# Kernel tuning notes

Hardware: AMD Instinct MI355X
Metric: run time of the kernel (lower is better)

## Reference

```python
import jax, jax.numpy as jnp
import numpy as np

B, N, FD = 2, 50000, 13
E = 250000
M, H = 128, 128          # message_dim, hidden_dim
EDGE_IN = 2 * FD + 8     # 34
NODE_IN = FD + 2 * M     # 269


def _mlp(x, w1, b1, w2, b2):
    return jnp.tanh(x @ w1 + b1) @ w2 + b2


def setup_inputs() -> dict:
    root = jax.random.key(0)
    k = lambda i: jax.random.fold_in(root, i)

    def lin(i, din, dout):
        w = jax.random.normal(k(i), (din, dout), jnp.float32) * np.float32(1.0 / np.sqrt(din))
        b = jax.random.normal(k(i + 100), (dout,), jnp.float32) * np.float32(0.01)
        return w, b

    ew1, eb1 = lin(1, EDGE_IN, H); ew2, eb2 = lin(2, H, M)      # mlp_edge
    ww1, wb1 = lin(3, EDGE_IN, H); ww2, wb2 = lin(4, H, 1)      # mlp_weight
    xw1, xb1 = lin(5, EDGE_IN, H); xw2, xb2 = lin(6, H, M)      # mlp_edge_world
    yw1, yb1 = lin(7, EDGE_IN, H); yw2, yb2 = lin(8, H, 1)      # mlp_weight_world
    nw1, nb1 = lin(9, NODE_IN, H); nw2, nb2 = lin(10, H, FD)    # mlp_node

    z_h = jax.random.normal(k(20), (B, N, FD), jnp.float32)
    edge_hh = jax.random.randint(k(21), (B, 2, E), 0, N, jnp.int32)
    edge_world = jax.random.randint(k(22), (B, 2, E), 0, N, jnp.int32)
    return dict(z_h=z_h, edge_hh=edge_hh, edge_world=edge_world,
                ew1=ew1, eb1=eb1, ew2=ew2, eb2=eb2,
                ww1=ww1, wb1=wb1, ww2=ww2, wb2=wb2,
                xw1=xw1, xb1=xb1, xw2=xw2, xb2=xb2,
                yw1=yw1, yb1=yb1, yw2=yw2, yb2=yb2,
                nw1=nw1, nb1=nb1, nw2=nw2, nb2=nb2)


def _edge_features(z, s, t):
    # z: (N, FD); s, t: (E,)
    pos, vel = z[:, 0:3], z[:, 3:6]
    diff = pos[s] - pos[t]                               # (E, 3)
    dist = jnp.sum(diff * diff, axis=-1, keepdims=True)  # (E, 1) squared distance
    vxc = jnp.cross(vel[s], vel[t])                      # (E, 3)
    vxn = jnp.linalg.norm(vxc, axis=-1, keepdims=True)   # (E, 1)
    return jnp.concatenate([diff, dist, vxc, vxn], axis=-1)  # (E, 8)


def reference(z_h, edge_hh, edge_world,
              ew1, eb1, ew2, eb2, ww1, wb1, ww2, wb2,
              xw1, xb1, xw2, xb2, yw1, yb1, yw2, yb2,
              nw1, nb1, nw2, nb2):
    n_nodes = z_h.shape[1]

    def per_batch(z, e_hh, e_w):
        # normal edges
        s, t = e_hh[0], e_hh[1]
        inp = jnp.concatenate([z[s], z[t], _edge_features(z, s, t)], axis=-1)  # (E, 34)
        m = _mlp(inp, ew1, eb1, ew2, eb2)                                       # (E, M)
        w = jax.nn.sigmoid(_mlp(inp, ww1, wb1, ww2, wb2))                       # (E, 1)
        agg_h = jnp.zeros((n_nodes, M), z.dtype).at[t].add(w * m)
        # world edges
        sw, tw = e_w[0], e_w[1]
        inpw = jnp.concatenate([z[sw], z[tw], _edge_features(z, sw, tw)], axis=-1)
        mw = _mlp(inpw, xw1, xb1, xw2, xb2)
        ww_ = jax.nn.sigmoid(_mlp(inpw, yw1, yb1, yw2, yb2))
        agg_w = jnp.zeros((n_nodes, M), z.dtype).at[tw].add(ww_ * mw)
        return agg_h, agg_w

    m_agg_h, m_agg_w = jax.vmap(per_batch)(z_h, edge_hh, edge_world)  # (B, N, M) each
    input_node = jnp.concatenate([z_h, m_agg_h, m_agg_w], axis=-1)    # (B, N, 269)
    delta_z_h = _mlp(input_node, nw1, nb1, nw2, nb2)                  # (B, N, 13)
    return delta_z_h
```

## Files before the change

kernel.cpp:

```cpp
#include <hip/hip_runtime.h>
#include <hip/hip_bf16.h>

#define B_   2
#define N_   50000
#define FD_  13
#define E_   250000
#define M_   128
#define H_   128

typedef __attribute__((ext_vector_type(8))) short  short8;
typedef __attribute__((ext_vector_type(8))) __bf16 bf16x8;
typedef __attribute__((ext_vector_type(4))) float  f32x4;
typedef __attribute__((ext_vector_type(4))) unsigned int uint4v;
typedef __attribute__((ext_vector_type(8))) unsigned short ushort8;

#define AGG_BYTES  (4ull * N_ * 128 * 4)
#define HIST_BYTES (4ull * N_ * 4)
#define SORT_BYTES (4ull * E_ * 4)
#define OFF_EW1 0u
#define OFF_WW1 8192u
#define OFF_EW2 16384u
#define OFF_XW1 32768u
#define OFF_YW1 40960u
#define OFF_XW2 49152u
#define OFF_NW1 65536u
#define OFF_NW2 102400u

__device__ __forceinline__ float bf2f(unsigned short u) {
    unsigned int v = ((unsigned int)u) << 16;
    return __builtin_bit_cast(float, v);
}
__device__ __forceinline__ unsigned short f2bf(float f) {
    __bf16 h = (__bf16)f;
    return __builtin_bit_cast(unsigned short, h);
}
__device__ __forceinline__ float tanh_fast(float x) {
    float e = __expf(x + x);
    float r = __builtin_amdgcn_rcpf(e + 1.0f);
    return __builtin_fmaf(-2.0f, r, 1.0f);
}
__device__ __forceinline__ float sigmoid_fast(float x) {
    return __builtin_amdgcn_rcpf(1.0f + __expf(-x));
}
__device__ __forceinline__ f32x4 mfma16(short8 a, short8 b, f32x4 c) {
    return __builtin_amdgcn_mfma_f32_16x16x32_bf16(
        __builtin_bit_cast(bf16x8, a), __builtin_bit_cast(bf16x8, b), c, 0, 0, 0);
}

__global__ void prep_kernel(const float* __restrict__ ew1, const float* __restrict__ ww1,
                            const float* __restrict__ ew2, const float* __restrict__ xw1,
                            const float* __restrict__ yw1, const float* __restrict__ xw2,
                            const float* __restrict__ nw1, const float* __restrict__ nw2,
                            unsigned short* __restrict__ fb, uint4v* __restrict__ hist4) {
    int m = blockIdx.y, f = blockIdx.x, l = threadIdx.x;
    {
        unsigned int flat = ((unsigned int)m * gridDim.x + (unsigned int)f) * 64u + (unsigned int)l;
        const uint4v zv = {0u, 0u, 0u, 0u};
        for (unsigned int i = flat; i < 50000u; i += gridDim.x * gridDim.y * 64u)
            hist4[i] = zv;
    }
    const float* src; int K, Nn, KS; unsigned int off;
    switch (m) {
        case 0: src = ew1; K = 34;  Nn = 128; KS = 2; off = OFF_EW1; break;
        case 1: src = ww1; K = 34;  Nn = 128; KS = 2; off = OFF_WW1; break;
        case 2: src = ew2; K = 128; Nn = 128; KS = 4; off = OFF_EW2; break;
        case 3: src = xw1; K = 34;  Nn = 128; KS = 2; off = OFF_XW1; break;
        case 4: src = yw1; K = 34;  Nn = 128; KS = 2; off = OFF_YW1; break;
        case 5: src = xw2; K = 128; Nn = 128; KS = 4; off = OFF_XW2; break;
        case 6: src = nw1; K = 269; Nn = 128; KS = 9; off = OFF_NW1; break;
        default: src = nw2; K = 128; Nn = 13; KS = 4; off = OFF_NW2; break;
    }
    int NT = (Nn + 15) / 16;
    if (f >= KS * NT) return;
    int ks = f / NT, nt = f % NT;
    int n = nt * 16 + (l & 15);
    unsigned short* dst = fb + off + ((unsigned int)f * 64u + (unsigned int)l) * 8u;
    #pragma unroll
    for (int j = 0; j < 8; j++) {
        int k = ks * 32 + ((l >> 4) * 8) + j;
        int kk = k; bool valid = (k < K) && (n < Nn);
        if (m == 6) {
            if (k < 256)      kk = k + 13;
            else if (k < 269) kk = k - 256;
            else              valid = false;
            valid = valid && (n < Nn);
        }
        dst[j] = valid ? f2bf(src[kk * Nn + n]) : (unsigned short)0;
    }
}

__global__ void hist_kernel(const int* __restrict__ ehh, const int* __restrict__ eww,
                            int* __restrict__ hist) {
    int p = blockIdx.y, idx = blockIdx.x * 256 + threadIdx.x;
    if (idx >= E_) return;
    const int* eg = ((p >> 1) ? eww : ehh) + (size_t)(p & 1) * 2 * E_;
    atomicAdd(&hist[p * N_ + eg[E_ + idx]], 1);
}

__global__ void scan_kernel(int* __restrict__ hist) {
    __shared__ int part[1024];
    const int p = blockIdx.x, tid = threadIdx.x;
    int* h = hist + p * N_;
    const int lo = tid * 52;
    int cnt = N_ - lo; if (cnt < 0) cnt = 0; if (cnt > 52) cnt = 52;
    int v[52];
    int sum = 0;
    if (cnt == 52) {
        const int4* src = (const int4*)(h + lo);
        #pragma unroll
        for (int i = 0; i < 13; i++) {
            int4 t = src[i];
            v[4*i] = t.x; v[4*i+1] = t.y; v[4*i+2] = t.z; v[4*i+3] = t.w;
        }
        #pragma unroll
        for (int i = 0; i < 52; i++) sum += v[i];
    } else {
        for (int i = 0; i < cnt; i++) sum += h[lo + i];
    }
    part[tid] = sum;
    __syncthreads();
    for (int off = 1; off < 1024; off <<= 1) {
        int t = (tid >= off) ? part[tid - off] : 0;
        __syncthreads();
        part[tid] += t;
        __syncthreads();
    }
    int excl = (tid == 0) ? 0 : part[tid - 1];
    if (cnt == 52) {
        int4* dst = (int4*)(h + lo);
        #pragma unroll
        for (int i = 0; i < 13; i++) {
            int4 o;
            o.x = excl; excl += v[4*i];
            o.y = excl; excl += v[4*i+1];
            o.z = excl; excl += v[4*i+2];
            o.w = excl; excl += v[4*i+3];
            dst[i] = o;
        }
    } else {
        for (int i = 0; i < cnt; i++) { int t = h[lo + i]; h[lo + i] = excl; excl += t; }
    }
}

__global__ void scatter_kernel(const int* __restrict__ ehh, const int* __restrict__ eww,
                               int* __restrict__ hist, unsigned int* __restrict__ sorted,
                               uint4v* __restrict__ agg4) {
    int p = blockIdx.y, idx = blockIdx.x * 256 + threadIdx.x;
    {
        unsigned int flat = ((unsigned int)p * gridDim.x + (unsigned int)blockIdx.x) * 256u
                          + (unsigned int)threadIdx.x;
        const unsigned int nthr = gridDim.x * gridDim.y * 256u;
        const uint4v zv = {0u, 0u, 0u, 0u};
        for (unsigned int i = flat; i < 6400000u; i += nthr) agg4[i] = zv;
    }
    if (idx >= E_) return;
    const int* eg = ((p >> 1) ? eww : ehh) + (size_t)(p & 1) * 2 * E_;
    int s = eg[idx];
    int t = eg[E_ + idx];
    int pos = atomicAdd(&hist[p * N_ + t], 1);
    sorted[(size_t)p * E_ + pos] = (unsigned int)s | ((unsigned int)t << 16);
}

__launch_bounds__(256, 3)
__global__ void edge_kernel_agg(const float* __restrict__ z,
                                const unsigned int* __restrict__ sorted,
                                const unsigned short* __restrict__ fb,
                                float* __restrict__ agg,
                                const float* __restrict__ eb1, const float* __restrict__ wb1,
                                const float* __restrict__ ww2, const float* __restrict__ wb2,
                                const float* __restrict__ eb2,
                                const float* __restrict__ xb1, const float* __restrict__ yb1,
                                const float* __restrict__ yw2, const float* __restrict__ yb2,
                                const float* __restrict__ xb2) {
    __shared__ alignas(16) unsigned short Abuf[128][48];
    __shared__ alignas(16) unsigned short Hbuf[128][136];
    __shared__ float w_acc[128];
    __shared__ int   tgt_s[128];

    const int tid  = threadIdx.x;
    const int lane = tid & 63, wv = tid >> 6, quad = lane >> 4, c = lane & 15;
    const int pass = blockIdx.y, b = pass & 1, set = pass >> 1;
    const int ebase = blockIdx.x * 128;

    const float* zb = z + (size_t)b * N_ * FD_;
    float* aggp = agg + (size_t)pass * N_ * 128;

    const short8* Fm1 = (const short8*)(fb + (set ? OFF_XW1 : OFF_EW1));
    const short8* Fw1 = (const short8*)(fb + (set ? OFF_YW1 : OFF_WW1));
    const short8* Fm2 = (const short8*)(fb + (set ? OFF_XW2 : OFF_EW2));
    const float* B1m = set ? xb1 : eb1;
    const float* B1w = set ? yb1 : wb1;
    const float* B2m = set ? xb2 : eb2;
    const float* Wv2 = set ? yw2 : ww2;
    const float wbias = (set ? yb2 : wb2)[0];

    const int nt0 = wv * 2;
    short8 bm[2][2], bw[2][2], b2f[2][4];
    float bias1m[2], bias1w[2], bias2m[2], w2v[2];
    #pragma unroll
    for (int i = 0; i < 2; i++) {
        int nt = nt0 + i, n = nt * 16 + c;
        #pragma unroll
        for (int ks = 0; ks < 2; ks++) { bm[i][ks] = Fm1[(ks * 8 + nt) * 64 + lane];
                                         bw[i][ks] = Fw1[(ks * 8 + nt) * 64 + lane]; }
        #pragma unroll
        for (int ks = 0; ks < 4; ks++) { b2f[i][ks] = Fm2[(ks * 8 + nt) * 64 + lane]; }
        bias1m[i] = B1m[n]; bias1w[i] = B1w[n];
        bias2m[i] = B2m[n]; w2v[i] = Wv2[n];
    }

    if (tid < 128) {
        const int e = tid;
        const int prt = e >> 4, pqd = (e >> 2) & 3, prr = e & 3;
        const int wpos = pqd * 32 + prt * 4 + prr;
        int sp = ebase + wpos;
        const bool valid = (sp < E_);
        if (!valid) sp = E_ - 1;
        unsigned int st = sorted[(size_t)pass * E_ + sp];
        int s = (int)(st & 0xffffu), t = (int)(st >> 16);
        tgt_s[e] = valid ? t : -1;
        w_acc[e] = 0.0f;
        const float* zs = zb + (size_t)s * 13;
        const float* zt = zb + (size_t)t * 13;
        float fs[13], ft[13];
        __builtin_memcpy(fs, zs, 13 * sizeof(float));
        __builtin_memcpy(ft, zt, 13 * sizeof(float));
        float d0 = fs[0] - ft[0], d1 = fs[1] - ft[1], d2 = fs[2] - ft[2];
        float dist = d0 * d0 + d1 * d1 + d2 * d2;
        float c0 = fs[4] * ft[5] - fs[5] * ft[4];
        float c1 = fs[5] * ft[3] - fs[3] * ft[5];
        float c2 = fs[3] * ft[4] - fs[4] * ft[3];
        float vxn = sqrtf(c0 * c0 + c1 * c1 + c2 * c2);
        unsigned short row[40];
        #pragma unroll
        for (int j = 0; j < 13; j++) { row[j] = f2bf(fs[j]); row[13 + j] = f2bf(ft[j]); }
        row[26] = f2bf(d0); row[27] = f2bf(d1); row[28] = f2bf(d2); row[29] = f2bf(dist);
        row[30] = f2bf(c0); row[31] = f2bf(c1); row[32] = f2bf(c2); row[33] = f2bf(vxn);
        #pragma unroll
        for (int j = 34; j < 40; j++) row[j] = 0;
        #pragma unroll
        for (int v = 0; v < 5; v++) {
            short8 sv;
            #pragma unroll
            for (int j = 0; j < 8; j++) sv[j] = (short)row[v * 8 + j];
            *((short8*)&Abuf[e][v * 8]) = sv;
        }
    }
    __syncthreads();

    #pragma unroll 1
    for (int rt = 0; rt < 8; rt++) {
        const unsigned short* ar = &Abuf[rt * 16 + c][0];
        short8 a0 = *((const short8*)(ar + quad * 8));
        short8 a1 = {};
        if (quad == 0) a1 = *((const short8*)(ar + 32));
        float wpart[4] = {0.f, 0.f, 0.f, 0.f};
        #pragma unroll
        for (int i = 0; i < 2; i++) {
            f32x4 accm = {bias1m[i], bias1m[i], bias1m[i], bias1m[i]};
            f32x4 accw = {bias1w[i], bias1w[i], bias1w[i], bias1w[i]};
            accm = mfma16(a0, bm[i][0], accm);
            accm = mfma16(a1, bm[i][1], accm);
            accw = mfma16(a0, bw[i][0], accw);
            accw = mfma16(a1, bw[i][1], accw);
            int n = (nt0 + i) * 16 + c;
            #pragma unroll
            for (int r = 0; r < 4; r++) {
                Hbuf[rt * 16 + quad * 4 + r][n] = f2bf(tanh_fast(accm[r]));
                wpart[r] += tanh_fast(accw[r]) * w2v[i];
            }
        }
        #pragma unroll
        for (int r = 0; r < 4; r++) {
            float v = wpart[r];
            v += __shfl_xor(v, 1); v += __shfl_xor(v, 2);
            v += __shfl_xor(v, 4); v += __shfl_xor(v, 8);
            if (c == r) atomicAdd(&w_acc[rt * 16 + quad * 4 + r], v);
        }
    }
    __syncthreads();
    if (tid < 128) w_acc[tid] = sigmoid_fast(w_acc[tid] + wbias);
    __syncthreads();

    {
        const int n0 = nt0 * 16 + c;
        const int n1 = n0 + 16;
        int   tp = -1;
        float va0 = 0.f, va1 = 0.f;
        bool  from_start = true;
        #pragma unroll 1
        for (int rt = 0; rt < 8; rt++) {
            const unsigned short* hr = &Hbuf[rt * 16 + c][0];
            short8 h0 = *((const short8*)(hr + quad * 8));
            short8 h1 = *((const short8*)(hr + 32 + quad * 8));
            short8 h2 = *((const short8*)(hr + 64 + quad * 8));
            short8 h3 = *((const short8*)(hr + 96 + quad * 8));
            f32x4 accA = {bias2m[0], bias2m[0], bias2m[0], bias2m[0]};
            f32x4 accB = {bias2m[1], bias2m[1], bias2m[1], bias2m[1]};
            accA = mfma16(h0, b2f[0][0], accA);
            accA = mfma16(h1, b2f[0][1], accA);
            accA = mfma16(h2, b2f[0][2], accA);
            accA = mfma16(h3, b2f[0][3], accA);
            accB = mfma16(h0, b2f[1][0], accB);
            accB = mfma16(h1, b2f[1][1], accB);
            accB = mfma16(h2, b2f[1][2], accB);
            accB = mfma16(h3, b2f[1][3], accB);
            const int elq = rt * 16 + quad * 4;
            #pragma unroll
            for (int r = 0; r < 4; r++) {
                const int row = elq + r;
                const int tg = tgt_s[row];
                const float g = w_acc[row];
                const float v0 = accA[r] * g;
                const float v1 = accB[r] * g;
                if (tg == tp) {
                    va0 += v0; va1 += v1;
                } else {
                    if (tp >= 0) {
                        float* dst = aggp + (size_t)tp * 128;
                        if (from_start) { atomicAdd(dst + n0, va0); atomicAdd(dst + n1, va1); }
                        else            { dst[n0] = va0; dst[n1] = va1; }
                    }
                    tp = tg; va0 = v0; va1 = v1;
                    from_start = (rt == 0 && r == 0);
                }
            }
        }
        if (tp >= 0) {
            float* dst = aggp + (size_t)tp * 128;
            atomicAdd(dst + n0, va0);
            atomicAdd(dst + n1, va1);
        }
    }
}

#define NODE_BLOCKS 1024
__launch_bounds__(256, 4)
__global__ void node_fused(const float* __restrict__ z,
                           const float* __restrict__ agg,
                           const unsigned short* __restrict__ fb,
                           const float* __restrict__ nb1,
                           const float* __restrict__ nb2,
                           float* __restrict__ out) {
    __shared__ alignas(16) unsigned short Abuf[2][16][296];
    __shared__ alignas(16) unsigned short Hbuf[16][136];

    const int tid  = threadIdx.x;
    const int lane = tid & 63, wv = tid >> 6, quad = lane >> 4, c = lane & 15;
    const int nl = tid >> 4, part = tid & 15;
    constexpr int NT_TILES = (B_ * N_) / 16;

    for (int j = tid; j < 2 * 16 * 19; j += 256) {
        int bufi = j / (16 * 19), jj = j % (16 * 19);
        Abuf[bufi][jj / 19][269 + jj % 19] = 0;
    }

    const short8* F1 = (const short8*)(fb + OFF_NW1);
    const short8* F2 = (const short8*)(fb + OFF_NW2);
    const int nt0 = wv * 2;
    const float b1a = nb1[nt0 * 16 + c];
    const float b1b = nb1[(nt0 + 1) * 16 + c];
    const float bias2 = (c < 13) ? nb2[c] : 0.0f;

    f32x4 pa0, pa1, pb0, pb1;
    float pz = 0.0f;

    int t = blockIdx.x;

    {
        const int g = t * 16 + nl;
        const int b = (g >= N_) ? 1 : 0;
        const int tt = g - b * N_;
        const float* ap0 = agg + ((size_t)b * N_ + tt) * 128 + part * 8;
        const float* ap1 = agg + ((size_t)(2 + b) * N_ + tt) * 128 + part * 8;
        pa0 = *(const f32x4*)(ap0); pa1 = *(const f32x4*)(ap0 + 4);
        pb0 = *(const f32x4*)(ap1); pb1 = *(const f32x4*)(ap1 + 4);
        if (tid < 208) pz = z[(size_t)(t * 16 + tid / 13) * 13 + (tid % 13)];
    }

    int buf = 0;
    for (; t < NT_TILES; t += NODE_BLOCKS) {
        const int g0 = t * 16;
        {
            ushort8 u;
            #pragma unroll
            for (int k = 0; k < 4; k++) { u[k] = f2bf(pa0[k]); u[4 + k] = f2bf(pa1[k]); }
            *((ushort8*)&Abuf[buf][nl][part * 8]) = u;
            #pragma unroll
            for (int k = 0; k < 4; k++) { u[k] = f2bf(pb0[k]); u[4 + k] = f2bf(pb1[k]); }
            *((ushort8*)&Abuf[buf][nl][128 + part * 8]) = u;
            if (tid < 208) Abuf[buf][tid / 13][256 + tid % 13] = f2bf(pz);
        }
        const int tn = t + NODE_BLOCKS;
        if (tn < NT_TILES) {
            const int g = tn * 16 + nl;
            const int b = (g >= N_) ? 1 : 0;
            const int tt = g - b * N_;
            const float* ap0 = agg + ((size_t)b * N_ + tt) * 128 + part * 8;
            const float* ap1 = agg + ((size_t)(2 + b) * N_ + tt) * 128 + part * 8;
            pa0 = *(const f32x4*)(ap0); pa1 = *(const f32x4*)(ap0 + 4);
            pb0 = *(const f32x4*)(ap1); pb1 = *(const f32x4*)(ap1 + 4);
            if (tid < 208) pz = z[(size_t)(tn * 16 + tid / 13) * 13 + (tid % 13)];
        }
        __syncthreads();

        {
            f32x4 acc0 = {b1a, b1a, b1a, b1a};
            f32x4 acc1 = {b1b, b1b, b1b, b1b};
            #pragma unroll
            for (int ks = 0; ks < 9; ks++) {
                short8 a = *((const short8*)(&Abuf[buf][c][0] + ks * 32 + quad * 8));
                acc0 = mfma16(a, F1[(ks * 8 + nt0) * 64 + lane], acc0);
                acc1 = mfma16(a, F1[(ks * 8 + nt0 + 1) * 64 + lane], acc1);
            }
            #pragma unroll
            for (int r = 0; r < 4; r++) {
                Hbuf[quad * 4 + r][nt0 * 16 + c]       = f2bf(tanh_fast(acc0[r]));
                Hbuf[quad * 4 + r][(nt0 + 1) * 16 + c] = f2bf(tanh_fast(acc1[r]));
            }
        }
        __syncthreads();

        if (wv == 0) {
            f32x4 acc = {bias2, bias2, bias2, bias2};
            #pragma unroll
            for (int ks = 0; ks < 4; ks++) {
                short8 h = *((const short8*)(&Hbuf[c][0] + ks * 32 + quad * 8));
                acc = mfma16(h, F2[ks * 64 + lane], acc);
            }
            #pragma unroll
            for (int r = 0; r < 4; r++) {
                int g = g0 + quad * 4 + r;
                if (c < 13) out[(size_t)g * 13 + c] = acc[r];
            }
        }
        buf ^= 1;
    }
}

extern "C" void kernel_launch(void* const* d_in, const int* in_sizes, int n_in,
                              void* d_out, int out_size, void* d_ws, size_t ws_size,
                              hipStream_t stream) {
    const float* z   = (const float*)d_in[0];
    const int* ehh   = (const int*)d_in[1];
    const int* eww   = (const int*)d_in[2];
    const float* ew1 = (const float*)d_in[3];
    const float* eb1 = (const float*)d_in[4];
    const float* ew2 = (const float*)d_in[5];
    const float* eb2 = (const float*)d_in[6];
    const float* ww1 = (const float*)d_in[7];
    const float* wb1 = (const float*)d_in[8];
    const float* ww2 = (const float*)d_in[9];
    const float* wb2 = (const float*)d_in[10];
    const float* xw1 = (const float*)d_in[11];
    const float* xb1 = (const float*)d_in[12];
    const float* xw2 = (const float*)d_in[13];
    const float* xb2 = (const float*)d_in[14];
    const float* yw1 = (const float*)d_in[15];
    const float* yb1 = (const float*)d_in[16];
    const float* yw2 = (const float*)d_in[17];
    const float* yb2 = (const float*)d_in[18];
    const float* nw1 = (const float*)d_in[19];
    const float* nb1 = (const float*)d_in[20];
    const float* nw2 = (const float*)d_in[21];
    const float* nb2 = (const float*)d_in[22];

    float* agg  = (float*)d_ws;
    int* hist   = (int*)((char*)d_ws + AGG_BYTES);
    unsigned int* sorted = (unsigned int*)((char*)d_ws + AGG_BYTES + HIST_BYTES);
    unsigned short* frag = (unsigned short*)((char*)d_ws + AGG_BYTES + HIST_BYTES + SORT_BYTES);

    prep_kernel<<<dim3(72, 8), 64, 0, stream>>>(ew1, ww1, ew2, xw1, yw1, xw2, nw1, nw2,
                                                frag, (uint4v*)hist);
    hist_kernel<<<dim3((E_ + 255) / 256, 4), 256, 0, stream>>>(ehh, eww, hist);
    scan_kernel<<<4, 1024, 0, stream>>>(hist);
    scatter_kernel<<<dim3((E_ + 255) / 256, 4), 256, 0, stream>>>(ehh, eww, hist, sorted,
                                                                  (uint4v*)agg);
    edge_kernel_agg<<<dim3((E_ + 127) / 128, 4), 256, 0, stream>>>(
        z, sorted, frag, agg,
        eb1, wb1, ww2, wb2, eb2,
        xb1, yb1, yw2, yb2, xb2);
    node_fused<<<NODE_BLOCKS, 256, 0, stream>>>(
        z, agg, frag, nb1, nb2, (float*)d_out);
}
```

Before: 399.9 us.

## Split edge kernel across eight waves with one output tile each

The edge aggregation kernel now runs 512 threads per block, and each of the 8 waves owns a single 16-column n-tile instead of two. This halves the per-thread weight fragments, accumulators and scatter accumulators, so more waves can be resident to hide gather and atomic latency. tanh and sigmoid also call exp2 directly with prescaled arguments instead of __expf. The risk is that the launch bound of 512 threads with 6 blocks forces a tight register budget that may cause spills, and more waves now contend on the shared-memory reductions and barriers.

```diff
diff --git a/kernel.cpp b/kernel.cpp
--- a/kernel.cpp
+++ b/kernel.cpp
@@ -35,12 +35,13 @@
     return __builtin_bit_cast(unsigned short, h);
 }
 __device__ __forceinline__ float tanh_fast(float x) {
-    float e = __expf(x + x);
+    float e = __builtin_amdgcn_exp2f(x * 2.8853900817779268f);
     float r = __builtin_amdgcn_rcpf(e + 1.0f);
     return __builtin_fmaf(-2.0f, r, 1.0f);
 }
 __device__ __forceinline__ float sigmoid_fast(float x) {
-    return __builtin_amdgcn_rcpf(1.0f + __expf(-x));
+    float e = __builtin_amdgcn_exp2f(x * -1.4426950408889634f);
+    return __builtin_amdgcn_rcpf(1.0f + e);
 }
 __device__ __forceinline__ f32x4 mfma16(short8 a, short8 b, f32x4 c) {
     return __builtin_amdgcn_mfma_f32_16x16x32_bf16(
@@ -161,7 +162,7 @@
     sorted[(size_t)p * E_ + pos] = (unsigned int)s | ((unsigned int)t << 16);
 }
 
-__launch_bounds__(256, 3)
+__launch_bounds__(512, 6)
 __global__ void edge_kernel_agg(const float* __restrict__ z,
                                 const unsigned int* __restrict__ sorted,
                                 const unsigned short* __restrict__ fb,
@@ -194,20 +195,16 @@
     const float* Wv2 = set ? yw2 : ww2;
     const float wbias = (set ? yb2 : wb2)[0];
 
-    const int nt0 = wv * 2;
-    short8 bm[2][2], bw[2][2], b2f[2][4];
-    float bias1m[2], bias1w[2], bias2m[2], w2v[2];
+    const int nt = wv;
+    const int n  = nt * 16 + c;
+    short8 bm[2], bw[2], b2f[4];
     #pragma unroll
-    for (int i = 0; i < 2; i++) {
-        int nt = nt0 + i, n = nt * 16 + c;
-        #pragma unroll
-        for (int ks = 0; ks < 2; ks++) { bm[i][ks] = Fm1[(ks * 8 + nt) * 64 + lane];
-                                         bw[i][ks] = Fw1[(ks * 8 + nt) * 64 + lane]; }
-        #pragma unroll
-        for (int ks = 0; ks < 4; ks++) { b2f[i][ks] = Fm2[(ks * 8 + nt) * 64 + lane]; }
-        bias1m[i] = B1m[n]; bias1w[i] = B1w[n];
-        bias2m[i] = B2m[n]; w2v[i] = Wv2[n];
-    }
+    for (int ks = 0; ks < 2; ks++) { bm[ks] = Fm1[(ks * 8 + nt) * 64 + lane];
+                                     bw[ks] = Fw1[(ks * 8 + nt) * 64 + lane]; }
+    #pragma unroll
+    for (int ks = 0; ks < 4; ks++) { b2f[ks] = Fm2[(ks * 8 + nt) * 64 + lane]; }
+    const float bias1m = B1m[n], bias1w = B1w[n];
+    const float bias2m = B2m[n], w2v = Wv2[n];
 
     if (tid < 128) {
         const int e = tid;
@@ -254,21 +251,17 @@
         short8 a0 = *((const short8*)(ar + quad * 8));
         short8 a1 = {};
         if (quad == 0) a1 = *((const short8*)(ar + 32));
-        float wpart[4] = {0.f, 0.f, 0.f, 0.f};
-        #pragma unroll
-        for (int i = 0; i < 2; i++) {
-            f32x4 accm = {bias1m[i], bias1m[i], bias1m[i], bias1m[i]};
-            f32x4 accw = {bias1w[i], bias1w[i], bias1w[i], bias1w[i]};
-            accm = mfma16(a0, bm[i][0], accm);
-            accm = mfma16(a1, bm[i][1], accm);
-            accw = mfma16(a0, bw[i][0], accw);
-            accw = mfma16(a1, bw[i][1], accw);
-            int n = (nt0 + i) * 16 + c;
-            #pragma unroll
-            for (int r = 0; r < 4; r++) {
-                Hbuf[rt * 16 + quad * 4 + r][n] = f2bf(tanh_fast(accm[r]));
-                wpart[r] += tanh_fast(accw[r]) * w2v[i];
-            }
+        f32x4 accm = {bias1m, bias1m, bias1m, bias1m};
+        f32x4 accw = {bias1w, bias1w, bias1w, bias1w};
+        accm = mfma16(a0, bm[0], accm);
+        accm = mfma16(a1, bm[1], accm);
+        accw = mfma16(a0, bw[0], accw);
+        accw = mfma16(a1, bw[1], accw);
+        float wpart[4];
+        #pragma unroll
+        for (int r = 0; r < 4; r++) {
+            Hbuf[rt * 16 + quad * 4 + r][n] = f2bf(tanh_fast(accm[r]));
+            wpart[r] = tanh_fast(accw[r]) * w2v;
         }
         #pragma unroll
         for (int r = 0; r < 4; r++) {
@@ -283,10 +276,9 @@
     __syncthreads();
 
     {
-        const int n0 = nt0 * 16 + c;
-        const int n1 = n0 + 16;
+        const int n0 = n;
         int   tp = -1;
-        float va0 = 0.f, va1 = 0.f;
+        float va = 0.f;
         bool  from_start = true;
         #pragma unroll 1
         for (int rt = 0; rt < 8; rt++) {
@@ -295,41 +287,33 @@
             short8 h1 = *((const short8*)(hr + 32 + quad * 8));
             short8 h2 = *((const short8*)(hr + 64 + quad * 8));
             short8 h3 = *((const short8*)(hr + 96 + quad * 8));
-            f32x4 accA = {bias2m[0], bias2m[0], bias2m[0], bias2m[0]};
-            f32x4 accB = {bias2m[1], bias2m[1], bias2m[1], bias2m[1]};
-            accA = mfma16(h0, b2f[0][0], accA);
-            accA = mfma16(h1, b2f[0][1], accA);
-            accA = mfma16(h2, b2f[0][2], accA);
-            accA = mfma16(h3, b2f[0][3], accA);
-            accB = mfma16(h0, b2f[1][0], accB);
-            accB = mfma16(h1, b2f[1][1], accB);
-            accB = mfma16(h2, b2f[1][2], accB);
-            accB = mfma16(h3, b2f[1][3], accB);
+            f32x4 acc = {bias2m, bias2m, bias2m, bias2m};
+            acc = mfma16(h0, b2f[0], acc);
+            acc = mfma16(h1, b2f[1], acc);
+            acc = mfma16(h2, b2f[2], acc);
+            acc = mfma16(h3, b2f[3], acc);
             const int elq = rt * 16 + quad * 4;
             #pragma unroll
             for (int r = 0; r < 4; r++) {
                 const int row = elq + r;
                 const int tg = tgt_s[row];
                 const float g = w_acc[row];
-                const float v0 = accA[r] * g;
-                const float v1 = accB[r] * g;
+                const float v = acc[r] * g;
                 if (tg == tp) {
-                    va0 += v0; va1 += v1;
+                    va += v;
                 } else {
                     if (tp >= 0) {
                         float* dst = aggp + (size_t)tp * 128;
-                        if (from_start) { atomicAdd(dst + n0, va0); atomicAdd(dst + n1, va1); }
-                        else            { dst[n0] = va0; dst[n1] = va1; }
+                        if (from_start) atomicAdd(dst + n0, va);
+                        else            dst[n0] = va;
                     }
-                    tp = tg; va0 = v0; va1 = v1;
+                    tp = tg; va = v;
                     from_start = (rt == 0 && r == 0);
                 }
             }
         }
         if (tp >= 0) {
-            float* dst = aggp + (size_t)tp * 128;
-            atomicAdd(dst + n0, va0);
-            atomicAdd(dst + n1, va1);
+            atomicAdd(aggp + (size_t)tp * 128 + n0, va);
         }
     }
 }
@@ -476,7 +460,7 @@
     scan_kernel<<<4, 1024, 0, stream>>>(hist);
     scatter_kernel<<<dim3((E_ + 255) / 256, 4), 256, 0, stream>>>(ehh, eww, hist, sorted,
                                                                   (uint4v*)agg);
-    edge_kernel_agg<<<dim3((E_ + 127) / 128, 4), 256, 0, stream>>>(
+    edge_kernel_agg<<<dim3((E_ + 127) / 128, 4), 512, 0, stream>>>(
         z, sorted, frag, agg,
         eb1, wb1, ww2, wb2, eb2,
         xb1, yb1, yw2, yb2, xb2);
```

Measured after the change: 426.9 us. 1.07x slower.
